# Performance work log

Hardware: AMD Instinct MI355X
Metric: run time of the kernel (lower is better)

## Reference

```python
import jax, jax.numpy as jnp
import numpy as np

N = 100000   # nodes
E = 1600000  # edges
G = 1000     # graphs in batch
F = 16       # in_features
D = 128      # embed_dim
C = 100      # num_centroid
K = 2        # num_class
L = 3        # num_layers


def setup_inputs() -> dict:
    key = jax.random.key(0)
    ks = jax.random.split(key, 8)
    x = jax.random.normal(ks[0], (N, F), dtype=jnp.float32)
    edge_index = jax.random.randint(ks[1], (2, E), 0, N)
    batch = jnp.sort(jax.random.randint(ks[2], (N,), 0, G))
    # learned params (xavier-like scaled, per init code)
    W_embed = jax.random.normal(ks[3], (D, F), dtype=jnp.float32) * 0.1
    W_convs = jax.random.normal(ks[4], (L, D, D), dtype=jnp.float32) * 0.05
    centroids = jax.random.normal(ks[5], (C, D), dtype=jnp.float32) * 0.1
    W_out = jax.random.normal(ks[6], (K, C), dtype=jnp.float32) * 0.1
    b_out = jax.random.uniform(ks[7], (K,), jnp.float32, -1e-4, 1e-4)
    return {"x": x, "edge_index": edge_index, "batch": batch,
            "W_embed": W_embed, "W_convs": W_convs, "centroids": centroids,
            "W_out": W_out, "b_out": b_out}


def _gcn_conv(h, W, src, dst, deg_isqrt):
    # h: [N, D]; standard GCNConv with self-loops, no bias
    m = h @ W.T                                   # [N, D]
    coef = deg_isqrt[src] * deg_isqrt[dst]        # [E+N]
    msg = m[src] * coef[:, None]                  # gather + scale
    return jax.ops.segment_sum(msg, dst, num_segments=N)


def reference(x, edge_index, batch, W_embed, W_convs, centroids, W_out, b_out):
    src0, dst0 = edge_index[0], edge_index[1]
    loop = jnp.arange(N, dtype=src0.dtype)
    src = jnp.concatenate([src0, loop])           # A + I edges
    dst = jnp.concatenate([dst0, loop])
    deg = jax.ops.segment_sum(jnp.ones(src.shape[0], jnp.float32), dst, num_segments=N)
    deg_isqrt = jax.lax.rsqrt(jnp.maximum(deg, 1.0))

    h = x @ W_embed.T                             # embedding, no bias
    for i in range(L):
        h = _gcn_conv(h, W_convs[i], src, dst, deg_isqrt)
        h = jax.nn.relu(h)                        # manifold (Euclidean) nonlinearity

    # centroid Euclidean distances: [N, C] via ||a-b||^2 = |a|^2 + |b|^2 - 2ab
    x2 = jnp.sum(h * h, axis=1, keepdims=True)            # [N,1]
    c2 = jnp.sum(centroids * centroids, axis=1)[None, :]  # [1,C]
    d2 = jnp.maximum(x2 + c2 - 2.0 * (h @ centroids.T), 0.0)
    dist = jnp.sqrt(d2 + 1e-12)                            # [N,C]

    # mean-pool per graph
    sums = jax.ops.segment_sum(dist, batch, num_segments=G)           # [G,C]
    cnts = jax.ops.segment_sum(jnp.ones((N,), jnp.float32), batch, num_segments=G)
    pooled = sums / jnp.maximum(cnts, 1.0)[:, None]

    return pooled @ W_out.T + b_out               # [G, K]
```

## Files before the change

kernel.cpp:

```cpp
#include <hip/hip_runtime.h>
#include <hip/hip_bf16.h>
#include <hip/hip_fp16.h>

constexpr int N_ = 100000;
constexpr int E_ = 1600000;
constexpr int G_ = 1000;
constexpr int D_ = 128;
constexpr int C_ = 100;
constexpr int K_ = 2;
constexpr int L_ = 3;
constexpr int NSB = (N_ + 255) / 256;
constexpr int NR_ = 8;
constexpr int RN_ = (N_ + NR_ - 1) / NR_;
constexpr int EPB_ = 1280;
constexpr int NCH_ = (E_ + EPB_ - 1) / EPB_;

using f16x8 = __attribute__((ext_vector_type(8))) _Float16;
using f16x4 = __attribute__((ext_vector_type(4))) _Float16;
using f32x4 = __attribute__((ext_vector_type(4))) float;

__global__ void init_ws(int* __restrict__ deg, int* __restrict__ cursor) {
    int i = blockIdx.x * 256 + threadIdx.x;
    if (i < N_) { deg[i] = 1; cursor[i] = 0; }
}

__global__ void count_deg(const int* __restrict__ dst, int* __restrict__ deg) {
    int e = blockIdx.x * 256 + threadIdx.x;
    if (e < E_) atomicAdd(&deg[dst[e]], 1);
}

__global__ void compute_disq(const int* __restrict__ deg, float* __restrict__ dis) {
    int i = blockIdx.x * 256 + threadIdx.x;
    if (i < N_) dis[i] = 1.0f / sqrtf((float)deg[i]);
}

__global__ void scan_block_sums(const int* __restrict__ deg, int* __restrict__ bsums) {
    __shared__ int sh[256];
    int i = blockIdx.x * 256 + threadIdx.x;
    int v = (i < N_) ? (deg[i] - 1) : 0;
    sh[threadIdx.x] = v;
    __syncthreads();
    for (int off = 128; off > 0; off >>= 1) {
        if (threadIdx.x < off) sh[threadIdx.x] += sh[threadIdx.x + off];
        __syncthreads();
    }
    if (threadIdx.x == 0) bsums[blockIdx.x] = sh[0];
}

__global__ void scan_offsets(int* __restrict__ bsums, int nb) {
    __shared__ int a[512], b[512];
    int t = threadIdx.x;
    int v = (t < nb) ? bsums[t] : 0;
    a[t] = v;
    __syncthreads();
    int* src = a; int* dst = b;
    for (int off = 1; off < 512; off <<= 1) {
        int x = src[t] + ((t >= off) ? src[t - off] : 0);
        dst[t] = x;
        __syncthreads();
        int* tmp = src; src = dst; dst = tmp;
    }
    if (t < nb) bsums[t] = src[t] - v;
}

__global__ void scan_write(const int* __restrict__ deg, const int* __restrict__ boffs,
                           int* __restrict__ rowp) {
    __shared__ int a[256], b[256];
    int t = threadIdx.x;
    int i = blockIdx.x * 256 + t;
    int v = (i < N_) ? (deg[i] - 1) : 0;
    a[t] = v;
    __syncthreads();
    int* src = a; int* dst = b;
    for (int off = 1; off < 256; off <<= 1) {
        int x = src[t] + ((t >= off) ? src[t - off] : 0);
        dst[t] = x;
        __syncthreads();
        int* tmp = src; src = dst; dst = tmp;
    }
    if (i < N_) rowp[i] = boffs[blockIdx.x] + src[t] - v;
    if (i == 0) rowp[N_] = E_;
}

__global__ __launch_bounds__(256) void fill_csr_xcd(
    const int* __restrict__ srcv, const int* __restrict__ dstv,
    const int* __restrict__ rowp, int* __restrict__ cursor,
    int* __restrict__ csr) {
    int r = blockIdx.x & 7;
    int chunk = blockIdx.x >> 3;
    int lo = r * RN_;
    int hi = lo + RN_;
    int ebeg = chunk * EPB_;
    int eend = ebeg + EPB_; if (eend > E_) eend = E_;
    for (int e = ebeg + threadIdx.x; e < eend; e += 256) {
        int d = dstv[e];
        if (d >= lo && d < hi) {
            int pos = atomicAdd(&cursor[d], 1);
            csr[rowp[d] + pos] = srcv[e];
        }
    }
}

__global__ __launch_bounds__(128) void embed_kernel(
    const float* __restrict__ x, const float* __restrict__ Wemb,
    _Float16* __restrict__ h) {
    __shared__ float4 xs[64 * 4];
    int t = threadIdx.x;
    float w[16];
#pragma unroll
    for (int f = 0; f < 16; ++f) w[f] = Wemb[t * 16 + f];
    int n0 = blockIdx.x * 64;
    const float4* x4 = (const float4*)x;
    for (int idx = t; idx < 64 * 4; idx += 128) {
        int gi = n0 * 4 + idx;
        xs[idx] = (gi < N_ * 4) ? x4[gi] : make_float4(0.f, 0.f, 0.f, 0.f);
    }
    __syncthreads();
    int lim = min(64, N_ - n0);
    for (int j = 0; j < lim; ++j) {
        float4 x0 = xs[j * 4 + 0], x1 = xs[j * 4 + 1];
        float4 x2 = xs[j * 4 + 2], x3 = xs[j * 4 + 3];
        float acc = x0.x * w[0] + x0.y * w[1] + x0.z * w[2] + x0.w * w[3]
                  + x1.x * w[4] + x1.y * w[5] + x1.z * w[6] + x1.w * w[7]
                  + x2.x * w[8] + x2.y * w[9] + x2.z * w[10] + x2.w * w[11]
                  + x3.x * w[12] + x3.y * w[13] + x3.z * w[14] + x3.w * w[15];
        h[(size_t)(n0 + j) * 128 + t] = (_Float16)acc;
    }
}

template<int FP16OUT>
__global__ __launch_bounds__(256) void mfma_gemm(
    const _Float16* __restrict__ h, const float* __restrict__ W,
    void* __restrict__ outp, int ncols, const float* __restrict__ dis) {
    int t = threadIdx.x;
    int w = t >> 6;
    int l = t & 63;
    int l15 = l & 15;
    int g = l >> 4;
    int nb0 = blockIdx.x * 128;

    f16x8 afr[2][4];
#pragma unroll
    for (int cg = 0; cg < 2; ++cg) {
        int c = 16 * w + 64 * cg + l15;
#pragma unroll
        for (int ks = 0; ks < 4; ++ks) {
            f16x8 af = {0, 0, 0, 0, 0, 0, 0, 0};
            if (c < ncols) {
                const float* wp = &W[c * 128 + 32 * ks + 8 * g];
                float4 w0 = *(const float4*)wp;
                float4 w1 = *(const float4*)(wp + 4);
                af[0] = (_Float16)w0.x; af[1] = (_Float16)w0.y;
                af[2] = (_Float16)w0.z; af[3] = (_Float16)w0.w;
                af[4] = (_Float16)w1.x; af[5] = (_Float16)w1.y;
                af[6] = (_Float16)w1.z; af[7] = (_Float16)w1.w;
            }
            afr[cg][ks] = af;
        }
    }

    for (int nt = 0; nt < 8; ++nt) {
        int nb = nb0 + 16 * nt;
        int node = nb + l15;
        int nodeL = node < N_ ? node : 0;
        f16x8 bfr[4];
#pragma unroll
        for (int ks = 0; ks < 4; ++ks)
            bfr[ks] = *(const f16x8*)&h[(size_t)nodeL * 128 + 32 * ks + 8 * g];
        f32x4 acc0 = {0.f, 0.f, 0.f, 0.f};
        f32x4 acc1 = {0.f, 0.f, 0.f, 0.f};
#pragma unroll
        for (int ks = 0; ks < 4; ++ks) {
            acc0 = __builtin_amdgcn_mfma_f32_16x16x32_f16(afr[0][ks], bfr[ks], acc0, 0, 0, 0);
            acc1 = __builtin_amdgcn_mfma_f32_16x16x32_f16(afr[1][ks], bfr[ks], acc1, 0, 0, 0);
        }
        if (node < N_) {
            int cb = 16 * w + 4 * g;
            if (FP16OUT) {
                float s = dis[node];
                ushort* mh = (ushort*)outp;
                __half2 p01 = __float22half2_rn(make_float2(acc0[0] * s, acc0[1] * s));
                __half2 p23 = __float22half2_rn(make_float2(acc0[2] * s, acc0[3] * s));
                uint2 u0;
                u0.x = *(unsigned int*)&p01; u0.y = *(unsigned int*)&p23;
                *(uint2*)&mh[(size_t)node * 128 + cb] = u0;
                __half2 q01 = __float22half2_rn(make_float2(acc1[0] * s, acc1[1] * s));
                __half2 q23 = __float22half2_rn(make_float2(acc1[2] * s, acc1[3] * s));
                uint2 u1;
                u1.x = *(unsigned int*)&q01; u1.y = *(unsigned int*)&q23;
                *(uint2*)&mh[(size_t)node * 128 + cb + 64] = u1;
            } else {
                float* o = (float*)outp;
                *(float4*)&o[(size_t)node * 128 + cb] =
                    make_float4(acc0[0], acc0[1], acc0[2], acc0[3]);
                *(float4*)&o[(size_t)node * 128 + cb + 64] =
                    make_float4(acc1[0], acc1[1], acc1[2], acc1[3]);
            }
        }
    }
}

__device__ inline float4 h4f4(uint2 u) {
    float2 fa = __half22float2(*(__half2*)&u.x);
    float2 fb = __half22float2(*(__half2*)&u.y);
    return make_float4(fa.x, fa.y, fb.x, fb.y);
}

__global__ __launch_bounds__(256) void aggregate(
    const ushort* __restrict__ mh, _Float16* __restrict__ hout,
    const int* __restrict__ rowp, const int* __restrict__ csr,
    const float* __restrict__ dis, float* __restrict__ x2out) {
    int t = threadIdx.x;
    int lane = t & 63;
    int l32 = lane & 31;
    int hbase = lane & 32;
    int node = blockIdx.x * 8 + ((t >> 6) << 1) + (hbase >> 5);
    const uint2* m2 = (const uint2*)mh;

    float4 acc0 = h4f4(m2[(size_t)node * 32 + l32]);
    float4 acc1 = make_float4(0.f, 0.f, 0.f, 0.f);
    int beg = rowp[node], end = rowp[node + 1];
    for (int base = beg; base < end; base += 32) {
        int cnt = end - base; if (cnt > 32) cnt = 32;
        int myidx = (l32 < cnt) ? csr[base + l32] : 0;
        int j = 0;
        for (; j + 8 <= cnt; j += 8) {
            int s0 = __shfl(myidx, hbase + j);
            int s1 = __shfl(myidx, hbase + j + 1);
            int s2 = __shfl(myidx, hbase + j + 2);
            int s3 = __shfl(myidx, hbase + j + 3);
            int s4 = __shfl(myidx, hbase + j + 4);
            int s5 = __shfl(myidx, hbase + j + 5);
            int s6 = __shfl(myidx, hbase + j + 6);
            int s7 = __shfl(myidx, hbase + j + 7);
            uint2 u0 = m2[(size_t)s0 * 32 + l32];
            uint2 u1 = m2[(size_t)s1 * 32 + l32];
            uint2 u2 = m2[(size_t)s2 * 32 + l32];
            uint2 u3 = m2[(size_t)s3 * 32 + l32];
            uint2 u4 = m2[(size_t)s4 * 32 + l32];
            uint2 u5 = m2[(size_t)s5 * 32 + l32];
            uint2 u6 = m2[(size_t)s6 * 32 + l32];
            uint2 u7 = m2[(size_t)s7 * 32 + l32];
            float4 v0 = h4f4(u0), v1 = h4f4(u1), v2 = h4f4(u2), v3 = h4f4(u3);
            float4 v4 = h4f4(u4), v5 = h4f4(u5), v6 = h4f4(u6), v7 = h4f4(u7);
            acc0.x += (v0.x + v1.x) + (v2.x + v3.x);
            acc0.y += (v0.y + v1.y) + (v2.y + v3.y);
            acc0.z += (v0.z + v1.z) + (v2.z + v3.z);
            acc0.w += (v0.w + v1.w) + (v2.w + v3.w);
            acc1.x += (v4.x + v5.x) + (v6.x + v7.x);
            acc1.y += (v4.y + v5.y) + (v6.y + v7.y);
            acc1.z += (v4.z + v5.z) + (v6.z + v7.z);
            acc1.w += (v4.w + v5.w) + (v6.w + v7.w);
        }
        for (; j + 4 <= cnt; j += 4) {
            int s0 = __shfl(myidx, hbase + j);
            int s1 = __shfl(myidx, hbase + j + 1);
            int s2 = __shfl(myidx, hbase + j + 2);
            int s3 = __shfl(myidx, hbase + j + 3);
            uint2 u0 = m2[(size_t)s0 * 32 + l32];
            uint2 u1 = m2[(size_t)s1 * 32 + l32];
            uint2 u2 = m2[(size_t)s2 * 32 + l32];
            uint2 u3 = m2[(size_t)s3 * 32 + l32];
            float4 v0 = h4f4(u0), v1 = h4f4(u1), v2 = h4f4(u2), v3 = h4f4(u3);
            acc0.x += (v0.x + v1.x) + (v2.x + v3.x);
            acc0.y += (v0.y + v1.y) + (v2.y + v3.y);
            acc0.z += (v0.z + v1.z) + (v2.z + v3.z);
            acc0.w += (v0.w + v1.w) + (v2.w + v3.w);
        }
        for (; j < cnt; ++j) {
            int s = __shfl(myidx, hbase + j);
            float4 v = h4f4(m2[(size_t)s * 32 + l32]);
            acc1.x += v.x; acc1.y += v.y; acc1.z += v.z; acc1.w += v.w;
        }
    }
    float di = dis[node];
    f16x4 hq;
    hq[0] = (_Float16)fmaxf(di * (acc0.x + acc1.x), 0.f);
    hq[1] = (_Float16)fmaxf(di * (acc0.y + acc1.y), 0.f);
    hq[2] = (_Float16)fmaxf(di * (acc0.z + acc1.z), 0.f);
    hq[3] = (_Float16)fmaxf(di * (acc0.w + acc1.w), 0.f);
    *(f16x4*)&hout[(size_t)node * 128 + (l32 << 2)] = hq;
    if (x2out) {
        float h0 = (float)hq[0], h1 = (float)hq[1];
        float h2 = (float)hq[2], h3 = (float)hq[3];
        float p = h0 * h0 + h1 * h1 + h2 * h2 + h3 * h3;
        p += __shfl_xor(p, 1);
        p += __shfl_xor(p, 2);
        p += __shfl_xor(p, 4);
        p += __shfl_xor(p, 8);
        p += __shfl_xor(p, 16);
        if (l32 == 0) x2out[node] = p;
    }
}

__global__ void c2_kernel(const float* __restrict__ cent, float* __restrict__ c2) {
    int c = blockIdx.x;
    int t = threadIdx.x;
    float v0 = (float)(_Float16)cent[c * 128 + t];
    float v1 = (float)(_Float16)cent[c * 128 + 64 + t];
    float p = v0 * v0 + v1 * v1;
    for (int off = 32; off > 0; off >>= 1) p += __shfl_down(p, off);
    if (t == 0) c2[c] = p;
}

__global__ __launch_bounds__(128) void pool_graph(
    const float* __restrict__ dots, const float* __restrict__ x2,
    const float* __restrict__ c2, const int* __restrict__ batch,
    float* __restrict__ pooled) {
    int g = blockIdx.x;
    int t = threadIdx.x;
    int lo = 0, hi = N_;
    while (lo < hi) { int mid = (lo + hi) >> 1; if (batch[mid] < g) lo = mid + 1; else hi = mid; }
    int s = lo;
    hi = N_;
    while (lo < hi) { int mid = (lo + hi) >> 1; if (batch[mid] < g + 1) lo = mid + 1; else hi = mid; }
    int e = lo;
    if (t >= C_) return;
    float cv = c2[t];
    float a0 = 0.f, a1 = 0.f, a2 = 0.f, a3 = 0.f;
    int n = s;
    for (; n + 4 <= e; n += 4) {
        float d0 = dots[(size_t)(n    ) * 128 + t];
        float d1 = dots[(size_t)(n + 1) * 128 + t];
        float d2 = dots[(size_t)(n + 2) * 128 + t];
        float d3 = dots[(size_t)(n + 3) * 128 + t];
        float x0 = x2[n], x1 = x2[n + 1], x2v = x2[n + 2], x3 = x2[n + 3];
        a0 += sqrtf(fmaxf(x0  + cv - 2.f * d0, 0.f) + 1e-12f);
        a1 += sqrtf(fmaxf(x1  + cv - 2.f * d1, 0.f) + 1e-12f);
        a2 += sqrtf(fmaxf(x2v + cv - 2.f * d2, 0.f) + 1e-12f);
        a3 += sqrtf(fmaxf(x3  + cv - 2.f * d3, 0.f) + 1e-12f);
    }
    for (; n < e; ++n) {
        float d = dots[(size_t)n * 128 + t];
        a0 += sqrtf(fmaxf(x2[n] + cv - 2.f * d, 0.f) + 1e-12f);
    }
    float inv = 1.0f / fmaxf((float)(e - s), 1.0f);
    pooled[g * C_ + t] = (a0 + a1 + a2 + a3) * inv;
}

__global__ void final_out(const float* __restrict__ pooled,
                          const float* __restrict__ W_out, const float* __restrict__ b_out,
                          float* __restrict__ out) {
    int i = blockIdx.x * 256 + threadIdx.x;
    if (i >= G_ * K_) return;
    int g = i >> 1, k = i & 1;
    float acc = 0.f;
    for (int c = 0; c < C_; ++c) acc += pooled[g * C_ + c] * W_out[k * C_ + c];
    out[i] = acc + b_out[k];
}

extern "C" void kernel_launch(void* const* d_in, const int* in_sizes, int n_in,
                              void* d_out, int out_size, void* d_ws, size_t ws_size,
                              hipStream_t stream) {
    const float* x       = (const float*)d_in[0];
    const int*   eidx    = (const int*)d_in[1];
    const int*   batch   = (const int*)d_in[2];
    const float* W_embed = (const float*)d_in[3];
    const float* W_convs = (const float*)d_in[4];
    const float* cent    = (const float*)d_in[5];
    const float* W_out   = (const float*)d_in[6];
    const float* b_out   = (const float*)d_in[7];
    float* out = (float*)d_out;

    char* p = (char*)d_ws;
    _Float16* h  = (_Float16*)p; p += (size_t)N_ * D_ * 2;
    float*  dots = (float*)p;  p += (size_t)N_ * D_ * 4;
    ushort* mh   = (ushort*)p; p += (size_t)N_ * D_ * 2;
    int*   deg  = (int*)p;   p += (size_t)N_ * 4;
    float* dis  = (float*)p; p += (size_t)N_ * 4;
    int*   rowp = (int*)p;   p += (size_t)(N_ + 2) * 4;
    int*   curs = (int*)p;   p += (size_t)N_ * 4;
    int*   csr  = (int*)p;   p += (size_t)E_ * 4;
    int*   bsum = (int*)p;   p += (size_t)512 * 4;
    float* c2   = (float*)p; p += (size_t)128 * 4;
    float* x2   = (float*)p; p += (size_t)N_ * 4;
    float* pool = (float*)p; p += (size_t)G_ * C_ * 4;

    const int* esrc = eidx;
    const int* edst = eidx + E_;

    init_ws<<<(N_ + 255) / 256, 256, 0, stream>>>(deg, curs);
    count_deg<<<(E_ + 255) / 256, 256, 0, stream>>>(edst, deg);
    compute_disq<<<(N_ + 255) / 256, 256, 0, stream>>>(deg, dis);
    scan_block_sums<<<NSB, 256, 0, stream>>>(deg, bsum);
    scan_offsets<<<1, 512, 0, stream>>>(bsum, NSB);
    scan_write<<<NSB, 256, 0, stream>>>(deg, bsum, rowp);
    fill_csr_xcd<<<NR_ * NCH_, 256, 0, stream>>>(esrc, edst, rowp, curs, csr);

    embed_kernel<<<(N_ + 63) / 64, 128, 0, stream>>>(x, W_embed, h);

    int ngb = (N_ + 127) / 128;
    for (int l = 0; l < L_; ++l) {
        mfma_gemm<1><<<ngb, 256, 0, stream>>>(h, W_convs + (size_t)l * D_ * D_,
                                              (void*)mh, 128, dis);
        aggregate<<<N_ / 8, 256, 0, stream>>>(mh, h, rowp, csr, dis,
                                              (l == L_ - 1) ? x2 : nullptr);
    }

    mfma_gemm<0><<<ngb, 256, 0, stream>>>(h, cent, (void*)dots, 100, nullptr);
    c2_kernel<<<C_, 64, 0, stream>>>(cent, c2);
    pool_graph<<<G_, 128, 0, stream>>>(dots, x2, c2, batch, pool);
    final_out<<<(G_ * K_ + 255) / 256, 256, 0, stream>>>(pool, W_out, b_out, out);
}
```

Baseline: 477.2 us.

## Fuse centroid distance GEMM with graph pooling and XCD-partition degree counting

The centroid GEMM now computes distances in registers and atomically accumulates them into per-graph pooled sums, so the N×128 fp32 dots buffer is never written or reread. The separate pool_graph kernel goes away, and the mean division moves into final_out. Degree counting is split by XCD node range to localize atomics. The init and disq kernels are replaced by memsets and folding into the scan. The trade-off is many float atomics on contended graph rows and nondeterministic summation order.

```diff
diff --git a/kernel.cpp b/kernel.cpp
--- a/kernel.cpp
+++ b/kernel.cpp
@@ -19,25 +19,26 @@
 using f16x4 = __attribute__((ext_vector_type(4))) _Float16;
 using f32x4 = __attribute__((ext_vector_type(4))) float;
 
-__global__ void init_ws(int* __restrict__ deg, int* __restrict__ cursor) {
-    int i = blockIdx.x * 256 + threadIdx.x;
-    if (i < N_) { deg[i] = 1; cursor[i] = 0; }
-}
-
-__global__ void count_deg(const int* __restrict__ dst, int* __restrict__ deg) {
-    int e = blockIdx.x * 256 + threadIdx.x;
-    if (e < E_) atomicAdd(&deg[dst[e]], 1);
-}
-
-__global__ void compute_disq(const int* __restrict__ deg, float* __restrict__ dis) {
-    int i = blockIdx.x * 256 + threadIdx.x;
-    if (i < N_) dis[i] = 1.0f / sqrtf((float)deg[i]);
-}
-
-__global__ void scan_block_sums(const int* __restrict__ deg, int* __restrict__ bsums) {
+__global__ __launch_bounds__(256) void count_deg_xcd(
+    const int* __restrict__ dstv, int* __restrict__ deg) {
+    int r = blockIdx.x & 7;
+    int chunk = blockIdx.x >> 3;
+    int lo = r * RN_;
+    int hi = lo + RN_;
+    int ebeg = chunk * EPB_;
+    int eend = ebeg + EPB_; if (eend > E_) eend = E_;
+    for (int e = ebeg + threadIdx.x; e < eend; e += 256) {
+        int d = dstv[e];
+        if (d >= lo && d < hi) atomicAdd(&deg[d], 1);
+    }
+}
+
+__global__ void scan_block_sums(const int* __restrict__ deg, int* __restrict__ bsums,
+                                float* __restrict__ dis) {
     __shared__ int sh[256];
     int i = blockIdx.x * 256 + threadIdx.x;
-    int v = (i < N_) ? (deg[i] - 1) : 0;
+    int v = (i < N_) ? deg[i] : 0;
+    if (i < N_) dis[i] = 1.0f / sqrtf((float)(v + 1));
     sh[threadIdx.x] = v;
     __syncthreads();
     for (int off = 128; off > 0; off >>= 1) {
@@ -68,7 +69,7 @@
     __shared__ int a[256], b[256];
     int t = threadIdx.x;
     int i = blockIdx.x * 256 + t;
-    int v = (i < N_) ? (deg[i] - 1) : 0;
+    int v = (i < N_) ? deg[i] : 0;
     a[t] = v;
     __syncthreads();
     int* src = a; int* dst = b;
@@ -128,10 +129,9 @@
     }
 }
 
-template<int FP16OUT>
 __global__ __launch_bounds__(256) void mfma_gemm(
     const _Float16* __restrict__ h, const float* __restrict__ W,
-    void* __restrict__ outp, int ncols, const float* __restrict__ dis) {
+    ushort* __restrict__ mh, const float* __restrict__ dis) {
     int t = threadIdx.x;
     int w = t >> 6;
     int l = t & 63;
@@ -145,9 +145,70 @@
         int c = 16 * w + 64 * cg + l15;
 #pragma unroll
         for (int ks = 0; ks < 4; ++ks) {
+            const float* wp = &W[c * 128 + 32 * ks + 8 * g];
+            float4 w0 = *(const float4*)wp;
+            float4 w1 = *(const float4*)(wp + 4);
+            f16x8 af;
+            af[0] = (_Float16)w0.x; af[1] = (_Float16)w0.y;
+            af[2] = (_Float16)w0.z; af[3] = (_Float16)w0.w;
+            af[4] = (_Float16)w1.x; af[5] = (_Float16)w1.y;
+            af[6] = (_Float16)w1.z; af[7] = (_Float16)w1.w;
+            afr[cg][ks] = af;
+        }
+    }
+
+    for (int nt = 0; nt < 8; ++nt) {
+        int nb = nb0 + 16 * nt;
+        int node = nb + l15;
+        int nodeL = node < N_ ? node : 0;
+        f16x8 bfr[4];
+#pragma unroll
+        for (int ks = 0; ks < 4; ++ks)
+            bfr[ks] = *(const f16x8*)&h[(size_t)nodeL * 128 + 32 * ks + 8 * g];
+        f32x4 acc0 = {0.f, 0.f, 0.f, 0.f};
+        f32x4 acc1 = {0.f, 0.f, 0.f, 0.f};
+#pragma unroll
+        for (int ks = 0; ks < 4; ++ks) {
+            acc0 = __builtin_amdgcn_mfma_f32_16x16x32_f16(afr[0][ks], bfr[ks], acc0, 0, 0, 0);
+            acc1 = __builtin_amdgcn_mfma_f32_16x16x32_f16(afr[1][ks], bfr[ks], acc1, 0, 0, 0);
+        }
+        if (node < N_) {
+            int cb = 16 * w + 4 * g;
+            float s = dis[node];
+            __half2 p01 = __float22half2_rn(make_float2(acc0[0] * s, acc0[1] * s));
+            __half2 p23 = __float22half2_rn(make_float2(acc0[2] * s, acc0[3] * s));
+            uint2 u0;
+            u0.x = *(unsigned int*)&p01; u0.y = *(unsigned int*)&p23;
+            *(uint2*)&mh[(size_t)node * 128 + cb] = u0;
+            __half2 q01 = __float22half2_rn(make_float2(acc1[0] * s, acc1[1] * s));
+            __half2 q23 = __float22half2_rn(make_float2(acc1[2] * s, acc1[3] * s));
+            uint2 u1;
+            u1.x = *(unsigned int*)&q01; u1.y = *(unsigned int*)&q23;
+            *(uint2*)&mh[(size_t)node * 128 + cb + 64] = u1;
+        }
+    }
+}
+
+__global__ __launch_bounds__(256) void mfma_dist_pool(
+    const _Float16* __restrict__ h, const float* __restrict__ cent,
+    const float* __restrict__ x2, const float* __restrict__ c2,
+    const int* __restrict__ batch, float* __restrict__ pooled) {
+    int t = threadIdx.x;
+    int w = t >> 6;
+    int l = t & 63;
+    int l15 = l & 15;
+    int g = l >> 4;
+    int nb0 = blockIdx.x * 128;
+
+    f16x8 afr[2][4];
+#pragma unroll
+    for (int cg = 0; cg < 2; ++cg) {
+        int c = 16 * w + 64 * cg + l15;
+#pragma unroll
+        for (int ks = 0; ks < 4; ++ks) {
             f16x8 af = {0, 0, 0, 0, 0, 0, 0, 0};
-            if (c < ncols) {
-                const float* wp = &W[c * 128 + 32 * ks + 8 * g];
+            if (c < C_) {
+                const float* wp = &cent[c * 128 + 32 * ks + 8 * g];
                 float4 w0 = *(const float4*)wp;
                 float4 w1 = *(const float4*)(wp + 4);
                 af[0] = (_Float16)w0.x; af[1] = (_Float16)w0.y;
@@ -176,25 +237,23 @@
         }
         if (node < N_) {
             int cb = 16 * w + 4 * g;
-            if (FP16OUT) {
-                float s = dis[node];
-                ushort* mh = (ushort*)outp;
-                __half2 p01 = __float22half2_rn(make_float2(acc0[0] * s, acc0[1] * s));
-                __half2 p23 = __float22half2_rn(make_float2(acc0[2] * s, acc0[3] * s));
-                uint2 u0;
-                u0.x = *(unsigned int*)&p01; u0.y = *(unsigned int*)&p23;
-                *(uint2*)&mh[(size_t)node * 128 + cb] = u0;
-                __half2 q01 = __float22half2_rn(make_float2(acc1[0] * s, acc1[1] * s));
-                __half2 q23 = __float22half2_rn(make_float2(acc1[2] * s, acc1[3] * s));
-                uint2 u1;
-                u1.x = *(unsigned int*)&q01; u1.y = *(unsigned int*)&q23;
-                *(uint2*)&mh[(size_t)node * 128 + cb + 64] = u1;
-            } else {
-                float* o = (float*)outp;
-                *(float4*)&o[(size_t)node * 128 + cb] =
-                    make_float4(acc0[0], acc0[1], acc0[2], acc0[3]);
-                *(float4*)&o[(size_t)node * 128 + cb + 64] =
-                    make_float4(acc1[0], acc1[1], acc1[2], acc1[3]);
+            float xv = x2[node];
+            int gb = batch[node];
+            float* prow = &pooled[(size_t)gb * C_];
+#pragma unroll
+            for (int j = 0; j < 4; ++j) {
+                float d2 = xv + c2[cb + j] - 2.0f * acc0[j];
+                float d = sqrtf(fmaxf(d2, 0.f) + 1e-12f);
+                atomicAdd(&prow[cb + j], d);
+            }
+            int c1 = cb + 64;
+            if (c1 < C_) {
+#pragma unroll
+                for (int j = 0; j < 4; ++j) {
+                    float d2 = xv + c2[c1 + j] - 2.0f * acc1[j];
+                    float d = sqrtf(fmaxf(d2, 0.f) + 1e-12f);
+                    atomicAdd(&prow[c1 + j], d);
+                }
             }
         }
     }
@@ -303,50 +362,23 @@
     if (t == 0) c2[c] = p;
 }
 
-__global__ __launch_bounds__(128) void pool_graph(
-    const float* __restrict__ dots, const float* __restrict__ x2,
-    const float* __restrict__ c2, const int* __restrict__ batch,
-    float* __restrict__ pooled) {
-    int g = blockIdx.x;
-    int t = threadIdx.x;
+__global__ void final_out(const float* __restrict__ pooled,
+                          const int* __restrict__ batch,
+                          const float* __restrict__ W_out, const float* __restrict__ b_out,
+                          float* __restrict__ out) {
+    int i = blockIdx.x * 256 + threadIdx.x;
+    if (i >= G_ * K_) return;
+    int g = i >> 1, k = i & 1;
     int lo = 0, hi = N_;
     while (lo < hi) { int mid = (lo + hi) >> 1; if (batch[mid] < g) lo = mid + 1; else hi = mid; }
     int s = lo;
     hi = N_;
     while (lo < hi) { int mid = (lo + hi) >> 1; if (batch[mid] < g + 1) lo = mid + 1; else hi = mid; }
     int e = lo;
-    if (t >= C_) return;
-    float cv = c2[t];
-    float a0 = 0.f, a1 = 0.f, a2 = 0.f, a3 = 0.f;
-    int n = s;
-    for (; n + 4 <= e; n += 4) {
-        float d0 = dots[(size_t)(n    ) * 128 + t];
-        float d1 = dots[(size_t)(n + 1) * 128 + t];
-        float d2 = dots[(size_t)(n + 2) * 128 + t];
-        float d3 = dots[(size_t)(n + 3) * 128 + t];
-        float x0 = x2[n], x1 = x2[n + 1], x2v = x2[n + 2], x3 = x2[n + 3];
-        a0 += sqrtf(fmaxf(x0  + cv - 2.f * d0, 0.f) + 1e-12f);
-        a1 += sqrtf(fmaxf(x1  + cv - 2.f * d1, 0.f) + 1e-12f);
-        a2 += sqrtf(fmaxf(x2v + cv - 2.f * d2, 0.f) + 1e-12f);
-        a3 += sqrtf(fmaxf(x3  + cv - 2.f * d3, 0.f) + 1e-12f);
-    }
-    for (; n < e; ++n) {
-        float d = dots[(size_t)n * 128 + t];
-        a0 += sqrtf(fmaxf(x2[n] + cv - 2.f * d, 0.f) + 1e-12f);
-    }
     float inv = 1.0f / fmaxf((float)(e - s), 1.0f);
-    pooled[g * C_ + t] = (a0 + a1 + a2 + a3) * inv;
-}
-
-__global__ void final_out(const float* __restrict__ pooled,
-                          const float* __restrict__ W_out, const float* __restrict__ b_out,
-                          float* __restrict__ out) {
-    int i = blockIdx.x * 256 + threadIdx.x;
-    if (i >= G_ * K_) return;
-    int g = i >> 1, k = i & 1;
     float acc = 0.f;
     for (int c = 0; c < C_; ++c) acc += pooled[g * C_ + c] * W_out[k * C_ + c];
-    out[i] = acc + b_out[k];
+    out[i] = acc * inv + b_out[k];
 }
 
 extern "C" void kernel_launch(void* const* d_in, const int* in_sizes, int n_in,
@@ -364,7 +396,6 @@
 
     char* p = (char*)d_ws;
     _Float16* h  = (_Float16*)p; p += (size_t)N_ * D_ * 2;
-    float*  dots = (float*)p;  p += (size_t)N_ * D_ * 4;
     ushort* mh   = (ushort*)p; p += (size_t)N_ * D_ * 2;
     int*   deg  = (int*)p;   p += (size_t)N_ * 4;
     float* dis  = (float*)p; p += (size_t)N_ * 4;
@@ -379,10 +410,12 @@
     const int* esrc = eidx;
     const int* edst = eidx + E_;
 
-    init_ws<<<(N_ + 255) / 256, 256, 0, stream>>>(deg, curs);
-    count_deg<<<(E_ + 255) / 256, 256, 0, stream>>>(edst, deg);
-    compute_disq<<<(N_ + 255) / 256, 256, 0, stream>>>(deg, dis);
-    scan_block_sums<<<NSB, 256, 0, stream>>>(deg, bsum);
+    hipMemsetAsync(deg, 0, (size_t)N_ * 4, stream);
+    hipMemsetAsync(curs, 0, (size_t)N_ * 4, stream);
+    hipMemsetAsync(pool, 0, (size_t)G_ * C_ * 4, stream);
+
+    count_deg_xcd<<<NR_ * NCH_, 256, 0, stream>>>(edst, deg);
+    scan_block_sums<<<NSB, 256, 0, stream>>>(deg, bsum, dis);
     scan_offsets<<<1, 512, 0, stream>>>(bsum, NSB);
     scan_write<<<NSB, 256, 0, stream>>>(deg, bsum, rowp);
     fill_csr_xcd<<<NR_ * NCH_, 256, 0, stream>>>(esrc, edst, rowp, curs, csr);
@@ -391,14 +424,12 @@
 
     int ngb = (N_ + 127) / 128;
     for (int l = 0; l < L_; ++l) {
-        mfma_gemm<1><<<ngb, 256, 0, stream>>>(h, W_convs + (size_t)l * D_ * D_,
-                                              (void*)mh, 128, dis);
+        mfma_gemm<<<ngb, 256, 0, stream>>>(h, W_convs + (size_t)l * D_ * D_, mh, dis);
         aggregate<<<N_ / 8, 256, 0, stream>>>(mh, h, rowp, csr, dis,
                                               (l == L_ - 1) ? x2 : nullptr);
     }
 
-    mfma_gemm<0><<<ngb, 256, 0, stream>>>(h, cent, (void*)dots, 100, nullptr);
     c2_kernel<<<C_, 64, 0, stream>>>(cent, c2);
-    pool_graph<<<G_, 128, 0, stream>>>(dots, x2, c2, batch, pool);
-    final_out<<<(G_ * K_ + 255) / 256, 256, 0, stream>>>(pool, W_out, b_out, out);
-}
+    mfma_dist_pool<<<ngb, 256, 0, stream>>>(h, cent, x2, c2, batch, pool);
+    final_out<<<(G_ * K_ + 255) / 256, 256, 0, stream>>>(pool, batch, W_out, b_out, out);
+}
```

After: 1.124 ms. 2.36x slower.
